# Kernel optimization log

Measured on AMD Instinct MI355X. Metric: run time of the kernel, lower is better.

Reference implementation:

```python
import jax, jax.numpy as jnp
import numpy as np

S = 7
B = 2
C = 20
LAMBDA_NOOBJ = 0.5
EPS = 1e-9  # guards IoU division; original divides by raw union


def setup_inputs() -> dict:
    key = jax.random.key(0)
    k1, k2 = jax.random.split(key)
    N = 8192
    preds = jax.random.uniform(k1, (N, S, S, B * (5 + C)), dtype=jnp.float32)
    targets = jax.random.uniform(k2, (N, S, S, B * (5 + C)), dtype=jnp.float32)
    return {"preds": preds, "targets": targets}


def _iou_xywh(a, b):
    # a, b: (..., 4) in (cx, cy, w, h); returns (...,) IoU
    ax1 = a[..., 0] - a[..., 2] / 2
    ay1 = a[..., 1] - a[..., 3] / 2
    ax2 = a[..., 0] + a[..., 2] / 2
    ay2 = a[..., 1] + a[..., 3] / 2
    bx1 = b[..., 0] - b[..., 2] / 2
    by1 = b[..., 1] - b[..., 3] / 2
    bx2 = b[..., 0] + b[..., 2] / 2
    by2 = b[..., 1] + b[..., 3] / 2
    iw = jnp.clip(jnp.minimum(ax2, bx2) - jnp.maximum(ax1, bx1), 0.0)
    ih = jnp.clip(jnp.minimum(ay2, by2) - jnp.maximum(ay1, by1), 0.0)
    inter = iw * ih
    union = a[..., 2] * a[..., 3] + b[..., 2] * b[..., 3] - inter
    return inter / (union + EPS)


def reference(preds, targets):
    N = preds.shape[0]
    p = preds.reshape(N, S, S, B, 5 + C)
    t = targets.reshape(N, S, S, B, 5 + C)

    # per-cell, per-slot IoU between pred box b and target box b: (N,S,S,B)
    ious = _iou_xywh(p[..., :4], t[..., :4])

    # best-box selection per cell
    best = jnp.argmax(ious, axis=-1)                       # (N,S,S)
    best_oh = jax.nn.one_hot(best, B, dtype=preds.dtype)   # (N,S,S,B)

    # object presence from target confidence of any box slot
    has_object = jnp.any(t[..., 4] > 0.0, axis=-1)         # (N,S,S)

    # 1) position loss (x,y) for the responsible box in object cells
    dxy = jnp.sum((p[..., 0:2] - t[..., 0:2]) ** 2, axis=-1)     # (N,S,S,B)
    pos_loss = jnp.sum(best_oh * dxy, axis=-1)                   # (N,S,S)
    loss = jnp.sum(jnp.where(has_object, pos_loss, 0.0))

    # 2) class loss (last C entries of the cell vector) for every cell
    pc = p[..., -1, 5:]   # (N,S,S,C)
    tc = t[..., -1, 5:]
    loss = loss + jnp.sum((pc - tc) ** 2)

    # 3) confidence loss: pred_conf = iou_b * p_class[gt], target_conf = iou_b
    gt_cls = jnp.argmax(tc, axis=-1)                                    # (N,S,S)
    p_gt = jnp.take_along_axis(pc, gt_cls[..., None], axis=-1)[..., 0]  # (N,S,S)
    conf_err = (ious * p_gt[..., None] - ious) ** 2                     # (N,S,S,B)
    w = jnp.where(best_oh > 0, 1.0, LAMBDA_NOOBJ)
    loss = loss + jnp.sum(w * conf_err)

    return loss / N
```

## Files before the change

kernel.cpp:

```cpp
#include <hip/hip_runtime.h>


#define NPC 50
#define CPT 32
#define TPB 64
#define TILE_F (CPT * NPC)

typedef const __attribute__((address_space(1))) void gvoid_t;
typedef __attribute__((address_space(3))) void lvoid_t;

__device__ __forceinline__ float iou_xywh(float px, float py, float pw, float ph,
                                          float tx, float ty, float tw, float th) {
    float ax1 = px - pw * 0.5f, ay1 = py - ph * 0.5f;
    float ax2 = px + pw * 0.5f, ay2 = py + ph * 0.5f;
    float bx1 = tx - tw * 0.5f, by1 = ty - th * 0.5f;
    float bx2 = tx + tw * 0.5f, by2 = ty + th * 0.5f;
    float iw = fmaxf(fminf(ax2, bx2) - fmaxf(ax1, bx1), 0.0f);
    float ih = fmaxf(fminf(ay2, by2) - fmaxf(ay1, by1), 0.0f);
    float inter = iw * ih;
    float uni = pw * ph + tw * th - inter;
    return inter / (uni + 1e-9f);
}

__device__ __forceinline__ float cell_loss(const float2* __restrict__ cp2,
                                           const float2* __restrict__ ct2) {
    float2 p01 = cp2[0], p23 = cp2[1];
    float2 t01 = ct2[0], t23 = ct2[1], t4_ = ct2[2];
    float2 pA = cp2[12], pB = cp2[13], pC = cp2[14];
    float2 tA = ct2[12], tB = ct2[13], tC = ct2[14];

    float iou0 = iou_xywh(p01.x, p01.y, p23.x, p23.y, t01.x, t01.y, t23.x, t23.y);
    float iou1 = iou_xywh(pA.y, pB.x, pB.y, pC.x, tA.y, tB.x, tB.y, tC.x);
    int best = (iou1 > iou0) ? 1 : 0;
    bool has_obj = (t4_.x > 0.0f) || (tC.y > 0.0f);

    float dx, dy;
    if (best == 0) { dx = p01.x - t01.x; dy = p01.y - t01.y; }
    else           { dx = pA.y - tA.y;   dy = pB.x - tB.x;   }
    float cell = has_obj ? (dx * dx + dy * dy) : 0.0f;

    float csum = 0.0f, bv = -1e30f, pg = 0.0f;
    #pragma unroll
    for (int j = 0; j < 10; ++j) {
        float2 tv = ct2[15 + j];
        float2 pv = cp2[15 + j];
        float d0 = pv.x - tv.x, d1 = pv.y - tv.y;
        csum += d0 * d0 + d1 * d1;
        if (tv.x > bv) { bv = tv.x; pg = pv.x; }
        if (tv.y > bv) { bv = tv.y; pg = pv.y; }
    }
    cell += csum;

    float f = pg - 1.0f, f2 = f * f;
    float e0 = iou0 * iou0 * f2, e1 = iou1 * iou1 * f2;
    cell += (best == 0) ? e0 : 0.5f * e0;
    cell += (best == 1) ? e1 : 0.5f * e1;
    return cell;
}

__global__ __launch_bounds__(TPB) void yolo_cell_kernel(
        const float* __restrict__ preds,
        const float* __restrict__ targets,
        float* __restrict__ part,
        int ncells, int nb) {
    __shared__ float lbuf[2][2 * TILE_F];

    const int lane = threadIdx.x;
    const int odd = lane & 1;
    const int c = lane >> 1;
    const int bid = blockIdx.x;
    const int ntiles = ncells / CPT;

    float acc = 0.0f;

    auto stage = [&](int b, int t) {
        const float* ps = preds + (long long)t * TILE_F;
        const float* ts = targets + (long long)t * TILE_F;
        float* lp = lbuf[b];
        float* lt = lbuf[b] + TILE_F;
        #pragma unroll
        for (int k = 0; k < 6; ++k)
            __builtin_amdgcn_global_load_lds((gvoid_t*)(ps + k * 256 + lane * 4),
                                             (lvoid_t*)(lp + k * 256), 16, 0, 0);
        __builtin_amdgcn_global_load_lds((gvoid_t*)(ps + 1536 + lane),
                                         (lvoid_t*)(lp + 1536), 4, 0, 0);
        #pragma unroll
        for (int k = 0; k < 6; ++k)
            __builtin_amdgcn_global_load_lds((gvoid_t*)(ts + k * 256 + lane * 4),
                                             (lvoid_t*)(lt + k * 256), 16, 0, 0);
        __builtin_amdgcn_global_load_lds((gvoid_t*)(ts + 1536 + lane),
                                         (lvoid_t*)(lt + 1536), 4, 0, 0);
    };

    if (bid < ntiles) stage(0, bid);
    int b = 0;
    for (int t = bid; t < ntiles; t += nb) {
        const int tn = t + nb;
        if (tn < ntiles) {
            stage(b ^ 1, tn);
            asm volatile("s_waitcnt vmcnt(14)" ::: "memory");
        } else {
            asm volatile("s_waitcnt vmcnt(0)" ::: "memory");
        }
        __builtin_amdgcn_sched_barrier(0);

        const float2* cp2 = (const float2*)(lbuf[b] + c * NPC);
        const float2* ct2 = (const float2*)(lbuf[b] + TILE_F + c * NPC);

        float iou0 = 0.0f, iou1 = 0.0f, dxy = 0.0f;
        int best = 0;
        bool has_obj = false;
        float csum = 0.0f, pg = 0.0f;
        if (!odd) {
            float2 p01 = cp2[0], p23 = cp2[1];
            float2 t01 = ct2[0], t23 = ct2[1], t4_ = ct2[2];
            float2 pA = cp2[12], pB = cp2[13], pC = cp2[14];
            float2 tA = ct2[12], tB = ct2[13], tC = ct2[14];
            iou0 = iou_xywh(p01.x, p01.y, p23.x, p23.y,
                            t01.x, t01.y, t23.x, t23.y);
            iou1 = iou_xywh(pA.y, pB.x, pB.y, pC.x,
                            tA.y, tB.x, tB.y, tC.x);
            best = (iou1 > iou0) ? 1 : 0;
            has_obj = (t4_.x > 0.0f) || (tC.y > 0.0f);
            float dx, dy;
            if (best == 0) { dx = p01.x - t01.x; dy = p01.y - t01.y; }
            else           { dx = pA.y - tA.y;   dy = pB.x - tB.x;   }
            dxy = dx * dx + dy * dy;
        } else {
            float bv = -1e30f;
            #pragma unroll
            for (int j = 0; j < 10; ++j) {
                float2 tv = ct2[15 + j];
                float2 pv = cp2[15 + j];
                float d0 = pv.x - tv.x, d1 = pv.y - tv.y;
                csum += d0 * d0 + d1 * d1;
                if (tv.x > bv) { bv = tv.x; pg = pv.x; }
                if (tv.y > bv) { bv = tv.y; pg = pv.y; }
            }
        }
        float pgx = __shfl_xor(pg, 1);
        float csx = __shfl_xor(csum, 1);
        if (!odd) {
            float cell = (has_obj ? dxy : 0.0f) + csx;
            float f = pgx - 1.0f, f2 = f * f;
            float e0 = iou0 * iou0 * f2, e1 = iou1 * iou1 * f2;
            cell += (best == 0) ? e0 : 0.5f * e0;
            cell += (best == 1) ? e1 : 0.5f * e1;
            acc += cell;
        }
        b ^= 1;
    }

    const int rem0 = ntiles * CPT;
    if (rem0 < ncells && bid == nb - 1) {
        for (int i = rem0 + lane; i < ncells; i += TPB) {
            const float2* cp2 = (const float2*)(preds + (long long)i * NPC);
            const float2* ct2 = (const float2*)(targets + (long long)i * NPC);
            acc += cell_loss(cp2, ct2);
        }
    }

    #pragma unroll
    for (int off = 32; off >= 1; off >>= 1) acc += __shfl_down(acc, off);
    if (lane == 0) part[bid] = acc;
}

__global__ __launch_bounds__(256) void yolo_final_kernel(
        const float* __restrict__ part, float* __restrict__ out,
        int nblk, float invN) {
    __shared__ float wsum[4];
    const int tid = threadIdx.x;
    float s = 0.0f;
    for (int i = tid; i < nblk; i += 256) s += part[i];
    #pragma unroll
    for (int off = 32; off >= 1; off >>= 1) s += __shfl_down(s, off);
    if ((tid & 63) == 0) wsum[tid >> 6] = s;
    __syncthreads();
    if (tid == 0) {
        out[0] = (wsum[0] + wsum[1] + wsum[2] + wsum[3]) * invN;
    }
}

extern "C" void kernel_launch(void* const* d_in, const int* in_sizes, int n_in,
                              void* d_out, int out_size, void* d_ws, size_t ws_size,
                              hipStream_t stream) {
    const float* preds = (const float*)d_in[0];
    const float* targets = (const float*)d_in[1];
    float* out = (float*)d_out;
    float* part = (float*)d_ws;

    const int ncells = in_sizes[0] / NPC;
    const int N = ncells / 49;
    const int nb = 1536;

    yolo_cell_kernel<<<nb, TPB, 0, stream>>>(preds, targets, part, ncells, nb);
    yolo_final_kernel<<<1, 256, 0, stream>>>(part, out, nb, 1.0f / (float)N);
}
```

Before: 32.82 us.

## Stage only needed bytes per cell via swizzled LDS layout, one cell per lane

Each tile now covers 64 cells, and every lane processes a full cell instead of pairs of lanes splitting one cell and exchanging results by shuffle. The staging loads copy only the 16-byte chunks that are used, into an XOR-swizzled LDS layout, plus a separate scalar load for the one confidence value that falls in an unloaded chunk. The goal is to avoid loading the unused class columns of the first box slot, spread LDS accesses across banks, and remove the cross-lane shuffle. The grid drops to 1024 blocks and the waitcnt is retuned to match the new load count. The chunk-offset arithmetic is intricate, so any mistake in it would silently give wrong values.

Measured after the change: 34.72 us. 1.06x slower.

```diff
diff --git a/kernel.cpp b/kernel.cpp
--- a/kernel.cpp
+++ b/kernel.cpp
@@ -2,9 +2,13 @@
 
 
 #define NPC 50
-#define CPT 32
+#define CPT 64
 #define TPB 64
 #define TILE_F (CPT * NPC)
+#define LP_F 2048
+#define LT_F 2048
+#define LE_F 64
+#define BUF_F (LP_F + LT_F + LE_F)
 
 typedef const __attribute__((address_space(1))) void gvoid_t;
 typedef __attribute__((address_space(3))) void lvoid_t;
@@ -63,34 +67,45 @@
         const float* __restrict__ targets,
         float* __restrict__ part,
         int ncells, int nb) {
-    __shared__ float lbuf[2][2 * TILE_F];
+    __shared__ float lbuf[2][BUF_F];
 
     const int lane = threadIdx.x;
-    const int odd = lane & 1;
-    const int c = lane >> 1;
     const int bid = blockIdx.x;
     const int ntiles = ncells / CPT;
 
+    unsigned goff[8];
+    {
+        const int pgrp = lane >> 4;
+        const int sig = lane & 15;
+        #pragma unroll
+        for (int i = 0; i < 8; ++i) {
+            const int q = 4 * i + pgrp;
+            const int s = sig ^ (q & 15);
+            const int kf = (s == 0) ? 0 : ((s <= 8) ? s + 5 : s + 9);
+            goff[i] = (unsigned)(q * 400 + kf * 16);
+        }
+    }
+    const unsigned eoff = (unsigned)((lane & 31) * 400 + 16);
+
+    auto stage = [&](int b, int t) {
+        const char* pb = (const char*)(preds + (long long)t * TILE_F);
+        const char* tb = (const char*)(targets + (long long)t * TILE_F);
+        float* lp = lbuf[b];
+        float* lt = lbuf[b] + LP_F;
+        float* le = lbuf[b] + LP_F + LT_F;
+        #pragma unroll
+        for (int i = 0; i < 8; ++i)
+            __builtin_amdgcn_global_load_lds((gvoid_t*)(pb + goff[i]),
+                                             (lvoid_t*)(lp + i * 256), 16, 0, 0);
+        #pragma unroll
+        for (int i = 0; i < 8; ++i)
+            __builtin_amdgcn_global_load_lds((gvoid_t*)(tb + goff[i]),
+                                             (lvoid_t*)(lt + i * 256), 16, 0, 0);
+        __builtin_amdgcn_global_load_lds((gvoid_t*)(tb + eoff),
+                                         (lvoid_t*)le, 4, 0, 0);
+    };
+
     float acc = 0.0f;
-
-    auto stage = [&](int b, int t) {
-        const float* ps = preds + (long long)t * TILE_F;
-        const float* ts = targets + (long long)t * TILE_F;
-        float* lp = lbuf[b];
-        float* lt = lbuf[b] + TILE_F;
-        #pragma unroll
-        for (int k = 0; k < 6; ++k)
-            __builtin_amdgcn_global_load_lds((gvoid_t*)(ps + k * 256 + lane * 4),
-                                             (lvoid_t*)(lp + k * 256), 16, 0, 0);
-        __builtin_amdgcn_global_load_lds((gvoid_t*)(ps + 1536 + lane),
-                                         (lvoid_t*)(lp + 1536), 4, 0, 0);
-        #pragma unroll
-        for (int k = 0; k < 6; ++k)
-            __builtin_amdgcn_global_load_lds((gvoid_t*)(ts + k * 256 + lane * 4),
-                                             (lvoid_t*)(lt + k * 256), 16, 0, 0);
-        __builtin_amdgcn_global_load_lds((gvoid_t*)(ts + 1536 + lane),
-                                         (lvoid_t*)(lt + 1536), 4, 0, 0);
-    };
 
     if (bid < ntiles) stage(0, bid);
     int b = 0;
@@ -98,56 +113,73 @@
         const int tn = t + nb;
         if (tn < ntiles) {
             stage(b ^ 1, tn);
-            asm volatile("s_waitcnt vmcnt(14)" ::: "memory");
+            asm volatile("s_waitcnt vmcnt(17)" ::: "memory");
         } else {
             asm volatile("s_waitcnt vmcnt(0)" ::: "memory");
         }
         __builtin_amdgcn_sched_barrier(0);
 
-        const float2* cp2 = (const float2*)(lbuf[b] + c * NPC);
-        const float2* ct2 = (const float2*)(lbuf[b] + TILE_F + c * NPC);
-
-        float iou0 = 0.0f, iou1 = 0.0f, dxy = 0.0f;
-        int best = 0;
-        bool has_obj = false;
-        float csum = 0.0f, pg = 0.0f;
-        if (!odd) {
-            float2 p01 = cp2[0], p23 = cp2[1];
-            float2 t01 = ct2[0], t23 = ct2[1], t4_ = ct2[2];
-            float2 pA = cp2[12], pB = cp2[13], pC = cp2[14];
-            float2 tA = ct2[12], tB = ct2[13], tC = ct2[14];
-            iou0 = iou_xywh(p01.x, p01.y, p23.x, p23.y,
-                            t01.x, t01.y, t23.x, t23.y);
-            iou1 = iou_xywh(pA.y, pB.x, pB.y, pC.x,
-                            tA.y, tB.x, tB.y, tC.x);
-            best = (iou1 > iou0) ? 1 : 0;
-            has_obj = (t4_.x > 0.0f) || (tC.y > 0.0f);
-            float dx, dy;
-            if (best == 0) { dx = p01.x - t01.x; dy = p01.y - t01.y; }
-            else           { dx = pA.y - tA.y;   dy = pB.x - tB.x;   }
-            dxy = dx * dx + dy * dy;
+        const float* lp = lbuf[b];
+        const float* lt = lbuf[b] + LP_F;
+        const float* le = lbuf[b] + LP_F + LT_F;
+        const int q = lane >> 1;
+        const int q15 = q & 15;
+        const float* lpq = lp + q * 64;
+        const float* ltq = lt + q * 64;
+#define S4(base, s) (*(const float4*)((base) + (((s) ^ q15) * 4)))
+
+        float csum = 0.0f, bv = -1e30f, pg = 0.0f;
+        auto cls4 = [&](float4 pv, float4 tv) {
+            float d;
+            d = pv.x - tv.x; csum += d * d; if (tv.x > bv) { bv = tv.x; pg = pv.x; }
+            d = pv.y - tv.y; csum += d * d; if (tv.y > bv) { bv = tv.y; pg = pv.y; }
+            d = pv.z - tv.z; csum += d * d; if (tv.z > bv) { bv = tv.z; pg = pv.z; }
+            d = pv.w - tv.w; csum += d * d; if (tv.w > bv) { bv = tv.w; pg = pv.w; }
+        };
+        auto cls1 = [&](float p, float t_) {
+            float d = p - t_; csum += d * d; if (t_ > bv) { bv = t_; pg = p; }
+        };
+
+        float iou0, iou1, dx, dy;
+        bool best, has_obj;
+        if (!(lane & 1)) {
+            float4 P0 = S4(lpq, 0), P1 = S4(lpq, 1), P2 = S4(lpq, 2);
+            float4 T0 = S4(ltq, 0), T1 = S4(ltq, 1), T2 = S4(ltq, 2);
+            iou0 = iou_xywh(P0.x, P0.y, P0.z, P0.w, T0.x, T0.y, T0.z, T0.w);
+            iou1 = iou_xywh(P1.y, P1.z, P1.w, P2.x, T1.y, T1.z, T1.w, T2.x);
+            has_obj = (le[q] > 0.0f) || (T2.y > 0.0f);
+            best = (iou1 > iou0);
+            dx = best ? P1.y - T1.y : P0.x - T0.x;
+            dy = best ? P1.z - T1.z : P0.y - T0.y;
+            cls1(P2.z, T2.z); cls1(P2.w, T2.w);
+            cls4(S4(lpq, 3), S4(ltq, 3));
+            cls4(S4(lpq, 4), S4(ltq, 4));
+            cls4(S4(lpq, 5), S4(ltq, 5));
+            cls4(S4(lpq, 6), S4(ltq, 6));
+            float4 P7 = S4(lpq, 7), T7 = S4(ltq, 7);
+            cls1(P7.x, T7.x); cls1(P7.y, T7.y);
         } else {
-            float bv = -1e30f;
-            #pragma unroll
-            for (int j = 0; j < 10; ++j) {
-                float2 tv = ct2[15 + j];
-                float2 pv = cp2[15 + j];
-                float d0 = pv.x - tv.x, d1 = pv.y - tv.y;
-                csum += d0 * d0 + d1 * d1;
-                if (tv.x > bv) { bv = tv.x; pg = pv.x; }
-                if (tv.y > bv) { bv = tv.y; pg = pv.y; }
-            }
-        }
-        float pgx = __shfl_xor(pg, 1);
-        float csx = __shfl_xor(csum, 1);
-        if (!odd) {
-            float cell = (has_obj ? dxy : 0.0f) + csx;
-            float f = pgx - 1.0f, f2 = f * f;
-            float e0 = iou0 * iou0 * f2, e1 = iou1 * iou1 * f2;
-            cell += (best == 0) ? e0 : 0.5f * e0;
-            cell += (best == 1) ? e1 : 0.5f * e1;
-            acc += cell;
-        }
+            float4 P7 = S4(lpq, 7), P8 = S4(lpq, 8), P9 = S4(lpq, 9), PA = S4(lpq, 10);
+            float4 T7 = S4(ltq, 7), T8 = S4(ltq, 8), T9 = S4(ltq, 9), TA = S4(ltq, 10);
+            iou0 = iou_xywh(P7.z, P7.w, P8.x, P8.y, T7.z, T7.w, T8.x, T8.y);
+            iou1 = iou_xywh(P9.w, PA.x, PA.y, PA.z, T9.w, TA.x, TA.y, TA.z);
+            has_obj = (T8.z > 0.0f) || (TA.w > 0.0f);
+            best = (iou1 > iou0);
+            dx = best ? P9.w - T9.w : P7.z - T7.z;
+            dy = best ? PA.x - TA.x : P7.w - T7.w;
+            cls4(S4(lpq, 11), S4(ltq, 11));
+            cls4(S4(lpq, 12), S4(ltq, 12));
+            cls4(S4(lpq, 13), S4(ltq, 13));
+            cls4(S4(lpq, 14), S4(ltq, 14));
+            cls4(S4(lpq, 15), S4(ltq, 15));
+        }
+#undef S4
+        float cell = (has_obj ? dx * dx + dy * dy : 0.0f) + csum;
+        float f = pg - 1.0f, f2 = f * f;
+        float e0 = iou0 * iou0 * f2, e1 = iou1 * iou1 * f2;
+        cell += best ? (0.5f * e0 + e1) : (e0 + 0.5f * e1);
+        acc += cell;
+
         b ^= 1;
     }
 
@@ -191,7 +223,7 @@
 
     const int ncells = in_sizes[0] / NPC;
     const int N = ncells / 49;
-    const int nb = 1536;
+    const int nb = 1024;
 
     yolo_cell_kernel<<<nb, TPB, 0, stream>>>(preds, targets, part, ncells, nb);
     yolo_final_kernel<<<1, 256, 0, stream>>>(part, out, nb, 1.0f / (float)N);
```
